# Kernel optimization log

Hardware: AMD Instinct MI355X
Metric: run time of the kernel (lower is better)

The kernel has to match this reference:

```python
import jax, jax.numpy as jnp
import numpy as np

NOISE_STD = 0.1
TOP_K = 2

def setup_inputs() -> dict:
    key = jax.random.key(0)
    k1, k2, k3, k4 = jax.random.split(key, 4)
    B, S, H = 4, 4096, 2048
    E, SE, NS = 64, 64, 10
    x = jax.random.normal(k1, (B, S, H), dtype=jnp.float32)
    scale_embeddings = jax.random.normal(k2, (NS, SE), dtype=jnp.float32)
    # nn.Linear(H+SE, E, bias=False) weight: [E, H+SE]
    router_w = jax.random.normal(k3, (E, H + SE), dtype=jnp.float32) / np.sqrt(H + SE).astype(np.float32)
    # pre-sampled standard-normal noise (training path), scaled by NOISE_STD inside reference
    noise = jax.random.normal(k4, (B, S, E), dtype=jnp.float32)
    return {"x": x, "scale_embeddings": scale_embeddings, "router_w": router_w,
            "noise": noise, "scale_idx": 3}

def reference(x, scale_embeddings, router_w, noise, scale_idx):
    B, S, _ = x.shape
    # scale_idx is not None branch: lookup one scale embedding, broadcast over tokens
    emb = scale_embeddings[scale_idx]                      # [SE]
    emb = jnp.broadcast_to(emb, (B, S, emb.shape[-1]))     # [B,S,SE]
    x_with_scale = jnp.concatenate([x, emb], axis=-1)      # [B,S,H+SE]
    # router: bias-free linear projection to expert logits
    router_logits = jnp.einsum('bsd,ed->bse', x_with_scale, router_w)
    router_logits = router_logits + noise * NOISE_STD      # training noise injection
    routing_probs = jax.nn.softmax(router_logits, axis=-1)  # [B,S,E]
    routing_weights, selected_experts = jax.lax.top_k(routing_probs, TOP_K)
    routing_weights = routing_weights / routing_weights.sum(axis=-1, keepdims=True)
    # scatter normalized weights into dense dispatch tensor [B,S,E]
    dispatch = (jax.nn.one_hot(selected_experts, routing_probs.shape[-1],
                               dtype=routing_probs.dtype)
                * routing_weights[..., None]).sum(axis=-2)
    return dispatch
```

## Files before the change

kernel.cpp:

```cpp
#include <hip/hip_runtime.h>
#include <hip/hip_bf16.h>
#include <math.h>
#include <stdint.h>


#define H_DIM 2048
#define K_TOTAL 2112
#define E_DIM 64
#define SE_DIM 64
#define NSTEP 64
#define TPB 32
#define NBLOCKS (16384 / TPB)
#define STEP_BYTES (12 * 1024)
#define WP_TOTAL (NSTEP * STEP_BYTES)
#define MINS(v) ((v) < NSTEP ? (v) : (NSTEP - 1))

typedef float  f32x4 __attribute__((ext_vector_type(4)));
typedef short  s16x8 __attribute__((ext_vector_type(8)));
typedef unsigned int u32x4 __attribute__((ext_vector_type(4)));

typedef uint32_t __attribute__((address_space(1))) gu32_t;
typedef uint32_t __attribute__((address_space(3))) lu32_t;
__device__ __forceinline__ void gload_lds16(const void* g, void* l) {
    __builtin_amdgcn_global_load_lds((const gu32_t*)g, (lu32_t*)l, 16, 0, 0);
}

__device__ __forceinline__ unsigned short bf16_rne(float f) {
    uint32_t u = __float_as_uint(f);
    return (unsigned short)((u + 0x7FFFu + ((u >> 16) & 1u)) >> 16);
}
__device__ __forceinline__ float bf16_f32(unsigned short h) {
    return __uint_as_float(((uint32_t)h) << 16);
}
__device__ __forceinline__ uint32_t bits_of_bf2(__hip_bfloat162 h) {
    uint32_t u; __builtin_memcpy(&u, &h, 4); return u;
}

__global__ void prep_kernel(const float* __restrict__ W,
                            const float* __restrict__ se,
                            const int* __restrict__ sidx,
                            unsigned short* __restrict__ Wp,
                            float* __restrict__ tail) {
    if (blockIdx.x == 64) {
        int e = threadIdx.x;
        if (e < 64) {
            const float* emb = se + (*sidx) * SE_DIM;
            float t = 0.f;
            for (int j = 0; j < SE_DIM; ++j)
                t = fmaf(emb[j], W[(size_t)e * K_TOTAL + H_DIM + j], t);
            tail[e] = t;
        }
        return;
    }
    int item = blockIdx.x * 256 + threadIdx.x;
    int lane = item & 63;
    int nt   = (item >> 6) & 3;
    int s    = item >> 8;
    int e     = nt * 16 + (lane & 15);
    int kbase = s * 32 + (lane >> 4) * 8;
    const float* wr = W + (size_t)e * K_TOTAL + kbase;
    unsigned short p0[8], p1[8], p2[8];
    #pragma unroll
    for (int j = 0; j < 8; ++j) {
        float v = wr[j];
        unsigned short a0 = bf16_rne(v);
        float r1 = v - bf16_f32(a0);
        unsigned short a1 = bf16_rne(r1);
        float r2 = r1 - bf16_f32(a1);
        p0[j] = a0; p1[j] = a1; p2[j] = bf16_rne(r2);
    }
    size_t rec = (size_t)s * 12 + nt * 3;
    unsigned short* d0 = Wp + (rec + 0) * 512 + lane * 8;
    unsigned short* d1 = Wp + (rec + 1) * 512 + lane * 8;
    unsigned short* d2 = Wp + (rec + 2) * 512 + lane * 8;
    #pragma unroll
    for (int j = 0; j < 8; ++j) { d0[j] = p0[j]; d1[j] = p1[j]; d2[j] = p2[j]; }
}

__device__ __forceinline__ void split3(const float4 fa, const float4 fb,
                                       s16x8& P0, s16x8& P1, s16x8& P2) {
    float f[8] = {fa.x, fa.y, fa.z, fa.w, fb.x, fb.y, fb.z, fb.w};
    uint32_t d0[4], d1[4], d2[4];
    #pragma unroll
    for (int p = 0; p < 4; ++p) {
        float v0 = f[2 * p], v1 = f[2 * p + 1];
        uint32_t u0 = bits_of_bf2(__float22bfloat162_rn(make_float2(v0, v1)));
        float r0 = v0 - __uint_as_float(u0 << 16);
        float r1 = v1 - __uint_as_float(u0 & 0xffff0000u);
        uint32_t u1 = bits_of_bf2(__float22bfloat162_rn(make_float2(r0, r1)));
        float s0 = r0 - __uint_as_float(u1 << 16);
        float s1 = r1 - __uint_as_float(u1 & 0xffff0000u);
        uint32_t u2 = bits_of_bf2(__float22bfloat162_rn(make_float2(s0, s1)));
        d0[p] = u0; d1[p] = u1; d2[p] = u2;
    }
    u32x4 q0 = {d0[0], d0[1], d0[2], d0[3]};
    u32x4 q1 = {d1[0], d1[1], d1[2], d1[3]};
    u32x4 q2 = {d2[0], d2[1], d2[2], d2[3]};
    __builtin_memcpy(&P0, &q0, 16);
    __builtin_memcpy(&P1, &q1, 16);
    __builtin_memcpy(&P2, &q2, 16);
}

__launch_bounds__(256, 2)
__global__ void router_kernel(const float* __restrict__ x,
                              const unsigned char* __restrict__ Wp,
                              const float* __restrict__ tail_g,
                              const float* __restrict__ noise,
                              float* __restrict__ out) {
    __shared__ __align__(16) unsigned char As[4][4096];
    __shared__ __align__(16) unsigned char Bs[4][STEP_BYTES];
    __shared__ float4 cand2[2][TPB];
    __shared__ float4 res[TPB];

    const int tid  = threadIdx.x;
    const int lane = tid & 63;
    const int wave = __builtin_amdgcn_readfirstlane(tid >> 6);
    const int mt   = wave >> 1;
    const int g    = wave & 1;
    const int tok0 = blockIdx.x * TPB;
    const int row  = lane & 15;
    const int quad = lane >> 4;
    const int c    = row;

    const int stok = tid >> 3;
    const int spos = tid & 7;
    const int schk = spos ^ (stok & 7);
    const float* asrc = x + (size_t)(tok0 + stok) * H_DIM + schk * 4;

    const int abase = (mt * 16 + row) * 128;
    const int aoff0 = abase + (((quad * 2)     ^ (row & 7)) << 4);
    const int aoff1 = abase + (((quad * 2 + 1) ^ (row & 7)) << 4);

    f32x4 acc0 = {0.f, 0.f, 0.f, 0.f}, acc1 = acc0;

    #define ISSUE_SET(s_, d_) do {                                          \
        const unsigned char* _bsrc = Wp + (size_t)(s_) * STEP_BYTES;        \
        gload_lds16(asrc + (size_t)(s_) * 32, &As[d_][tid * 16]);           \
        gload_lds16(_bsrc + (size_t)tid * 16,          &Bs[d_][tid * 16]);          \
        gload_lds16(_bsrc + (size_t)(tid + 256) * 16,  &Bs[d_][(tid + 256) * 16]);  \
        gload_lds16(_bsrc + (size_t)(tid + 512) * 16,  &Bs[d_][(tid + 512) * 16]);  \
    } while (0)

    ISSUE_SET(0, 0);
    ISSUE_SET(1, 1);
    ISSUE_SET(2, 2);

    for (int s = 0; s < NSTEP; ++s) {
        asm volatile("s_waitcnt vmcnt(8)\n\ts_barrier" ::: "memory");

        const int slot = s & 3;
        const float4* ab = (const float4*)&As[slot][0];
        float4 a0 = *(const float4*)((const unsigned char*)ab + aoff0);
        float4 a1 = *(const float4*)((const unsigned char*)ab + aoff1);
        s16x8 A0, A1, A2;
        split3(a0, a1, A0, A1, A2);

        const unsigned char* base = &Bs[slot][g * 6144 + lane * 16];
        #pragma unroll
        for (int nt = 0; nt < 2; ++nt) {
            s16x8 B0 = *(const s16x8*)(base + (nt * 3 + 0) * 1024);
            s16x8 B1 = *(const s16x8*)(base + (nt * 3 + 1) * 1024);
            s16x8 B2 = *(const s16x8*)(base + (nt * 3 + 2) * 1024);
            f32x4 a = nt ? acc1 : acc0;
            a = __builtin_amdgcn_mfma_f32_16x16x32_bf16(A0, B0, a, 0, 0, 0);
            a = __builtin_amdgcn_mfma_f32_16x16x32_bf16(A0, B1, a, 0, 0, 0);
            a = __builtin_amdgcn_mfma_f32_16x16x32_bf16(A1, B0, a, 0, 0, 0);
            a = __builtin_amdgcn_mfma_f32_16x16x32_bf16(A0, B2, a, 0, 0, 0);
            a = __builtin_amdgcn_mfma_f32_16x16x32_bf16(A1, B1, a, 0, 0, 0);
            a = __builtin_amdgcn_mfma_f32_16x16x32_bf16(A2, B0, a, 0, 0, 0);
            if (nt) acc1 = a; else acc0 = a;
        }

        ISSUE_SET(MINS(s + 3), (s + 3) & 3);
    }
    #undef ISSUE_SET

    float tl0 = tail_g[g * 32 + c], tl1 = tail_g[g * 32 + 16 + c];
    #pragma unroll
    for (int r = 0; r < 4; ++r) {
        const int tl = mt * 16 + quad * 4 + r;
        const float* nz = noise + (size_t)(tok0 + tl) * E_DIM + g * 32;
        float v0 = acc0[r] + tl0 + 0.1f * nz[c];
        float v1 = acc1[r] + tl1 + 0.1f * nz[16 + c];
        float V1, V2; int I1, I2;
        if (v1 > v0) { V1 = v1; I1 = g * 32 + 16 + c; V2 = v0; I2 = g * 32 + c; }
        else         { V1 = v0; I1 = g * 32 + c;      V2 = v1; I2 = g * 32 + 16 + c; }
        #pragma unroll
        for (int m = 8; m; m >>= 1) {
            float o1 = __shfl_xor(V1, m, 64); int oi1 = __shfl_xor(I1, m, 64);
            float o2 = __shfl_xor(V2, m, 64); int oi2 = __shfl_xor(I2, m, 64);
            if (o1 > V1 || (o1 == V1 && oi1 < I1)) {
                float nv2; int ni2;
                if (V1 > o2 || (V1 == o2 && I1 < oi2)) { nv2 = V1; ni2 = I1; }
                else                                   { nv2 = o2; ni2 = oi2; }
                V1 = o1; I1 = oi1; V2 = nv2; I2 = ni2;
            } else {
                if (o1 > V2 || (o1 == V2 && oi1 < I2)) { V2 = o1; I2 = oi1; }
            }
        }
        if (c == r)
            cand2[g][tl] = make_float4(V1, __int_as_float(I1), V2, __int_as_float(I2));
    }
    __syncthreads();

    if (tid < TPB) {
        float4 q0 = cand2[0][tid];
        float4 q1 = cand2[1][tid];
        float V1 = q0.x, V2 = q0.z;
        int   I1 = __float_as_int(q0.y), I2 = __float_as_int(q0.w);
        if (q1.x > V1) {
            if (q1.z > V1) { V2 = q1.z; I2 = __float_as_int(q1.w); }
            else           { V2 = V1;   I2 = I1; }
            V1 = q1.x; I1 = __float_as_int(q1.y);
        } else if (q1.x > V2) {
            V2 = q1.x; I2 = __float_as_int(q1.y);
        }
        float d   = expf(V2 - V1);
        float inv = 1.0f / (1.0f + d);
        res[tid] = make_float4(inv, __int_as_float(I1), d * inv, __int_as_float(I2));
    }
    __syncthreads();

    float4* outb = (float4*)out + (size_t)blockIdx.x * (TPB * E_DIM / 4);
    #pragma unroll
    for (int pp = 0; pp < 2; ++pp) {
        int p = tid + pp * 256;
        int t = p >> 4, cc = p & 15;
        float4 rr = res[t];
        int ri1 = __float_as_int(rr.y), ri2 = __float_as_int(rr.w);
        int e = cc * 4;
        float4 o;
        o.x = (e + 0 == ri1) ? rr.x : (e + 0 == ri2) ? rr.z : 0.0f;
        o.y = (e + 1 == ri1) ? rr.x : (e + 1 == ri2) ? rr.z : 0.0f;
        o.z = (e + 2 == ri1) ? rr.x : (e + 2 == ri2) ? rr.z : 0.0f;
        o.w = (e + 3 == ri1) ? rr.x : (e + 3 == ri2) ? rr.z : 0.0f;
        outb[p] = o;
    }
}

extern "C" void kernel_launch(void* const* d_in, const int* in_sizes, int n_in,
                              void* d_out, int out_size, void* d_ws, size_t ws_size,
                              hipStream_t stream) {
    const float* x     = (const float*)d_in[0];
    const float* se    = (const float*)d_in[1];
    const float* W     = (const float*)d_in[2];
    const float* noise = (const float*)d_in[3];
    const int*   sidx  = (const int*)d_in[4];
    float* out = (float*)d_out;

    unsigned short* Wp   = (unsigned short*)d_ws;
    float*          tail = (float*)((char*)d_ws + WP_TOTAL);

    hipLaunchKernelGGL(prep_kernel, dim3(65), dim3(256), 0, stream, W, se, sidx, Wp, tail);
    hipLaunchKernelGGL(router_kernel, dim3(NBLOCKS), dim3(256), 0, stream,
                       x, (const unsigned char*)Wp, tail, noise, out);
}
```

Baseline: 223.9 us.

## Split expert columns across 8 waves and issue prefetch before compute

Doubles the block to 512 threads, so each wave owns one 16-expert column tile instead of two. The A and B staging buffers merge into one 16KB set per stage, loaded with two global-to-LDS loads per thread. The prefetch for step s+3 now goes out right after the barrier instead of after the MFMAs, and the wait count drops to match. Top-2 selection merges four per-wave candidates instead of two. The aim is more parallel waves and better latency hiding, at the cost of more block-wide barriers per token and the same data traffic.

Result: slower. 241.3 us (+7.8%).

```diff
diff --git a/kernel.cpp b/kernel.cpp
--- a/kernel.cpp
+++ b/kernel.cpp
@@ -12,6 +12,7 @@
 #define TPB 32
 #define NBLOCKS (16384 / TPB)
 #define STEP_BYTES (12 * 1024)
+#define SET_BYTES (16 * 1024)
 #define WP_TOTAL (NSTEP * STEP_BYTES)
 #define MINS(v) ((v) < NSTEP ? (v) : (NSTEP - 1))
 
@@ -101,44 +102,49 @@
     __builtin_memcpy(&P2, &q2, 16);
 }
 
-__launch_bounds__(256, 2)
+__launch_bounds__(512, 4)
 __global__ void router_kernel(const float* __restrict__ x,
                               const unsigned char* __restrict__ Wp,
                               const float* __restrict__ tail_g,
                               const float* __restrict__ noise,
                               float* __restrict__ out) {
-    __shared__ __align__(16) unsigned char As[4][4096];
-    __shared__ __align__(16) unsigned char Bs[4][STEP_BYTES];
-    __shared__ float4 cand2[2][TPB];
+    __shared__ __align__(16) unsigned char S[4][SET_BYTES];
+    __shared__ float4 cand[4][TPB];
     __shared__ float4 res[TPB];
 
     const int tid  = threadIdx.x;
     const int lane = tid & 63;
     const int wave = __builtin_amdgcn_readfirstlane(tid >> 6);
-    const int mt   = wave >> 1;
-    const int g    = wave & 1;
+    const int mt   = wave >> 2;
+    const int g    = wave & 3;
     const int tok0 = blockIdx.x * TPB;
     const int row  = lane & 15;
     const int quad = lane >> 4;
     const int c    = row;
 
-    const int stok = tid >> 3;
-    const int spos = tid & 7;
-    const int schk = spos ^ (stok & 7);
-    const float* asrc = x + (size_t)(tok0 + stok) * H_DIM + schk * 4;
+    const char* s1; size_t str1;
+    if (tid < 256) {
+        int st = tid >> 3, sp = tid & 7;
+        s1 = (const char*)(x + (size_t)(tok0 + st) * H_DIM + ((sp ^ (st & 7)) << 2));
+        str1 = 128;
+    } else {
+        s1 = (const char*)Wp + (size_t)(tid - 256) * 16;
+        str1 = STEP_BYTES;
+    }
+    const char* s2 = (const char*)Wp + (size_t)(tid + 256) * 16;
+    const int d1 = tid * 16;
+    const int d2 = tid * 16 + 8192;
 
     const int abase = (mt * 16 + row) * 128;
     const int aoff0 = abase + (((quad * 2)     ^ (row & 7)) << 4);
     const int aoff1 = abase + (((quad * 2 + 1) ^ (row & 7)) << 4);
-
-    f32x4 acc0 = {0.f, 0.f, 0.f, 0.f}, acc1 = acc0;
-
-    #define ISSUE_SET(s_, d_) do {                                          \
-        const unsigned char* _bsrc = Wp + (size_t)(s_) * STEP_BYTES;        \
-        gload_lds16(asrc + (size_t)(s_) * 32, &As[d_][tid * 16]);           \
-        gload_lds16(_bsrc + (size_t)tid * 16,          &Bs[d_][tid * 16]);          \
-        gload_lds16(_bsrc + (size_t)(tid + 256) * 16,  &Bs[d_][(tid + 256) * 16]);  \
-        gload_lds16(_bsrc + (size_t)(tid + 512) * 16,  &Bs[d_][(tid + 512) * 16]);  \
+    const int boff  = 4096 + g * 3072 + lane * 16;
+
+    f32x4 acc = {0.f, 0.f, 0.f, 0.f};
+
+    #define ISSUE_SET(s_, d_) do {                                  \
+        gload_lds16(s1 + (size_t)(s_) * str1,       &S[d_][d1]);    \
+        gload_lds16(s2 + (size_t)(s_) * STEP_BYTES, &S[d_][d2]);    \
     } while (0)
 
     ISSUE_SET(0, 0);
@@ -146,45 +152,37 @@
     ISSUE_SET(2, 2);
 
     for (int s = 0; s < NSTEP; ++s) {
-        asm volatile("s_waitcnt vmcnt(8)\n\ts_barrier" ::: "memory");
-
-        const int slot = s & 3;
-        const float4* ab = (const float4*)&As[slot][0];
-        float4 a0 = *(const float4*)((const unsigned char*)ab + aoff0);
-        float4 a1 = *(const float4*)((const unsigned char*)ab + aoff1);
+        asm volatile("s_waitcnt vmcnt(4)\n\ts_barrier" ::: "memory");
+
+        ISSUE_SET(MINS(s + 3), (s + 3) & 3);
+
+        const unsigned char* sb = &S[s & 3][0];
+        float4 a0 = *(const float4*)(sb + aoff0);
+        float4 a1 = *(const float4*)(sb + aoff1);
         s16x8 A0, A1, A2;
         split3(a0, a1, A0, A1, A2);
 
-        const unsigned char* base = &Bs[slot][g * 6144 + lane * 16];
-        #pragma unroll
-        for (int nt = 0; nt < 2; ++nt) {
-            s16x8 B0 = *(const s16x8*)(base + (nt * 3 + 0) * 1024);
-            s16x8 B1 = *(const s16x8*)(base + (nt * 3 + 1) * 1024);
-            s16x8 B2 = *(const s16x8*)(base + (nt * 3 + 2) * 1024);
-            f32x4 a = nt ? acc1 : acc0;
-            a = __builtin_amdgcn_mfma_f32_16x16x32_bf16(A0, B0, a, 0, 0, 0);
-            a = __builtin_amdgcn_mfma_f32_16x16x32_bf16(A0, B1, a, 0, 0, 0);
-            a = __builtin_amdgcn_mfma_f32_16x16x32_bf16(A1, B0, a, 0, 0, 0);
-            a = __builtin_amdgcn_mfma_f32_16x16x32_bf16(A0, B2, a, 0, 0, 0);
-            a = __builtin_amdgcn_mfma_f32_16x16x32_bf16(A1, B1, a, 0, 0, 0);
-            a = __builtin_amdgcn_mfma_f32_16x16x32_bf16(A2, B0, a, 0, 0, 0);
-            if (nt) acc1 = a; else acc0 = a;
-        }
-
-        ISSUE_SET(MINS(s + 3), (s + 3) & 3);
+        const unsigned char* bb = sb + boff;
+        s16x8 B0 = *(const s16x8*)(bb);
+        s16x8 B1 = *(const s16x8*)(bb + 1024);
+        s16x8 B2 = *(const s16x8*)(bb + 2048);
+        acc = __builtin_amdgcn_mfma_f32_16x16x32_bf16(A0, B0, acc, 0, 0, 0);
+        acc = __builtin_amdgcn_mfma_f32_16x16x32_bf16(A0, B1, acc, 0, 0, 0);
+        acc = __builtin_amdgcn_mfma_f32_16x16x32_bf16(A1, B0, acc, 0, 0, 0);
+        acc = __builtin_amdgcn_mfma_f32_16x16x32_bf16(A0, B2, acc, 0, 0, 0);
+        acc = __builtin_amdgcn_mfma_f32_16x16x32_bf16(A1, B1, acc, 0, 0, 0);
+        acc = __builtin_amdgcn_mfma_f32_16x16x32_bf16(A2, B0, acc, 0, 0, 0);
     }
     #undef ISSUE_SET
 
-    float tl0 = tail_g[g * 32 + c], tl1 = tail_g[g * 32 + 16 + c];
+    float tl = tail_g[g * 16 + c];
     #pragma unroll
     for (int r = 0; r < 4; ++r) {
-        const int tl = mt * 16 + quad * 4 + r;
-        const float* nz = noise + (size_t)(tok0 + tl) * E_DIM + g * 32;
-        float v0 = acc0[r] + tl0 + 0.1f * nz[c];
-        float v1 = acc1[r] + tl1 + 0.1f * nz[16 + c];
-        float V1, V2; int I1, I2;
-        if (v1 > v0) { V1 = v1; I1 = g * 32 + 16 + c; V2 = v0; I2 = g * 32 + c; }
-        else         { V1 = v0; I1 = g * 32 + c;      V2 = v1; I2 = g * 32 + 16 + c; }
+        const int tlk = mt * 16 + quad * 4 + r;
+        const float* nz = noise + (size_t)(tok0 + tlk) * E_DIM + g * 16;
+        float v = acc[r] + tl + 0.1f * nz[c];
+        float V1 = v, V2 = -3.4e38f;
+        int   I1 = g * 16 + c, I2 = 0x7fffffff;
         #pragma unroll
         for (int m = 8; m; m >>= 1) {
             float o1 = __shfl_xor(V1, m, 64); int oi1 = __shfl_xor(I1, m, 64);
@@ -199,21 +197,26 @@
             }
         }
         if (c == r)
-            cand2[g][tl] = make_float4(V1, __int_as_float(I1), V2, __int_as_float(I2));
+            cand[g][tlk] = make_float4(V1, __int_as_float(I1), V2, __int_as_float(I2));
     }
     __syncthreads();
 
     if (tid < TPB) {
-        float4 q0 = cand2[0][tid];
-        float4 q1 = cand2[1][tid];
+        float4 q0 = cand[0][tid];
         float V1 = q0.x, V2 = q0.z;
         int   I1 = __float_as_int(q0.y), I2 = __float_as_int(q0.w);
-        if (q1.x > V1) {
-            if (q1.z > V1) { V2 = q1.z; I2 = __float_as_int(q1.w); }
-            else           { V2 = V1;   I2 = I1; }
-            V1 = q1.x; I1 = __float_as_int(q1.y);
-        } else if (q1.x > V2) {
-            V2 = q1.x; I2 = __float_as_int(q1.y);
+        #pragma unroll
+        for (int j = 1; j < 4; ++j) {
+            float4 qj = cand[j][tid];
+            float o1 = qj.x, o2 = qj.z;
+            int  oi1 = __float_as_int(qj.y), oi2 = __float_as_int(qj.w);
+            if (o1 > V1) {
+                if (o2 > V1) { V2 = o2; I2 = oi2; }
+                else         { V2 = V1; I2 = I1;  }
+                V1 = o1; I1 = oi1;
+            } else if (o1 > V2) {
+                V2 = o1; I2 = oi1;
+            }
         }
         float d   = expf(V2 - V1);
         float inv = 1.0f / (1.0f + d);
@@ -222,10 +225,8 @@
     __syncthreads();
 
     float4* outb = (float4*)out + (size_t)blockIdx.x * (TPB * E_DIM / 4);
-    #pragma unroll
-    for (int pp = 0; pp < 2; ++pp) {
-        int p = tid + pp * 256;
-        int t = p >> 4, cc = p & 15;
+    {
+        int t = tid >> 4, cc = tid & 15;
         float4 rr = res[t];
         int ri1 = __float_as_int(rr.y), ri2 = __float_as_int(rr.w);
         int e = cc * 4;
@@ -234,7 +235,7 @@
         o.y = (e + 1 == ri1) ? rr.x : (e + 1 == ri2) ? rr.z : 0.0f;
         o.z = (e + 2 == ri1) ? rr.x : (e + 2 == ri2) ? rr.z : 0.0f;
         o.w = (e + 3 == ri1) ? rr.x : (e + 3 == ri2) ? rr.z : 0.0f;
-        outb[p] = o;
+        outb[tid] = o;
     }
 }
 
@@ -252,6 +253,6 @@
     float*          tail = (float*)((char*)d_ws + WP_TOTAL);
 
     hipLaunchKernelGGL(prep_kernel, dim3(65), dim3(256), 0, stream, W, se, sidx, Wp, tail);
-    hipLaunchKernelGGL(router_kernel, dim3(NBLOCKS), dim3(256), 0, stream,
+    hipLaunchKernelGGL(router_kernel, dim3(NBLOCKS), dim3(512), 0, stream,
                        x, (const unsigned char*)Wp, tail, noise, out);
 }
```

## Restructure LDS pipeline into three-slot ring with split-phase loads and setprio

Applied to the files above, without the earlier changes.

Replaces the four-deep separate A/B LDS buffers with a three-slot combined ring and splits each K-step into two phases. The second weight half is issued after the first MFMA group, with barriers and waitcnts placed between the phases. The weight prepack reorders N-tiles so that each phase reads a contiguous region. It also raises wave priority around the MFMA chains, aiming to cut LDS footprint for occupancy and to overlap loads with compute more finely. The cost is an extra barrier per step and a shallower prefetch depth.

After: 279.2 us. 1.25x slower.

```diff
diff --git a/kernel.cpp b/kernel.cpp
--- a/kernel.cpp
+++ b/kernel.cpp
@@ -12,6 +12,7 @@
 #define TPB 32
 #define NBLOCKS (16384 / TPB)
 #define STEP_BYTES (12 * 1024)
+#define SET_BYTES (16 * 1024)
 #define WP_TOTAL (NSTEP * STEP_BYTES)
 #define MINS(v) ((v) < NSTEP ? (v) : (NSTEP - 1))
 
@@ -69,7 +70,8 @@
         float r2 = r1 - bf16_f32(a1);
         p0[j] = a0; p1[j] = a1; p2[j] = bf16_rne(r2);
     }
-    size_t rec = (size_t)s * 12 + nt * 3;
+    int slot = ((nt & 1) << 1) | (nt >> 1);
+    size_t rec = (size_t)s * 12 + slot * 3;
     unsigned short* d0 = Wp + (rec + 0) * 512 + lane * 8;
     unsigned short* d1 = Wp + (rec + 1) * 512 + lane * 8;
     unsigned short* d2 = Wp + (rec + 2) * 512 + lane * 8;
@@ -107,8 +109,7 @@
                               const float* __restrict__ tail_g,
                               const float* __restrict__ noise,
                               float* __restrict__ out) {
-    __shared__ __align__(16) unsigned char As[4][4096];
-    __shared__ __align__(16) unsigned char Bs[4][STEP_BYTES];
+    __shared__ __align__(16) unsigned char S[3][SET_BYTES];
     __shared__ float4 cand2[2][TPB];
     __shared__ float4 res[TPB];
 
@@ -126,6 +127,7 @@
     const int spos = tid & 7;
     const int schk = spos ^ (stok & 7);
     const float* asrc = x + (size_t)(tok0 + stok) * H_DIM + schk * 4;
+    const unsigned char* bsrc = Wp + (size_t)tid * 16;
 
     const int abase = (mt * 16 + row) * 128;
     const int aoff0 = abase + (((quad * 2)     ^ (row & 7)) << 4);
@@ -133,47 +135,66 @@
 
     f32x4 acc0 = {0.f, 0.f, 0.f, 0.f}, acc1 = acc0;
 
-    #define ISSUE_SET(s_, d_) do {                                          \
-        const unsigned char* _bsrc = Wp + (size_t)(s_) * STEP_BYTES;        \
-        gload_lds16(asrc + (size_t)(s_) * 32, &As[d_][tid * 16]);           \
-        gload_lds16(_bsrc + (size_t)tid * 16,          &Bs[d_][tid * 16]);          \
-        gload_lds16(_bsrc + (size_t)(tid + 256) * 16,  &Bs[d_][(tid + 256) * 16]);  \
-        gload_lds16(_bsrc + (size_t)(tid + 512) * 16,  &Bs[d_][(tid + 512) * 16]);  \
+    #define ISSUE_P0(s_, d_) do {                                       \
+        const unsigned char* _b = bsrc + (size_t)(s_) * STEP_BYTES;     \
+        gload_lds16(asrc + (size_t)(s_) * 32, &S[d_][tid * 16]);        \
+        gload_lds16(_b,        &S[d_][4096 + tid * 16]);                \
+        gload_lds16(_b + 4096, &S[d_][8192 + tid * 16]);                \
     } while (0)
-
-    ISSUE_SET(0, 0);
-    ISSUE_SET(1, 1);
-    ISSUE_SET(2, 2);
-
+    #define ISSUE_P1(s_, d_)                                            \
+        gload_lds16(bsrc + (size_t)(s_) * STEP_BYTES + 8192,            \
+                    &S[d_][12288 + tid * 16])
+
+    ISSUE_P0(0, 0); ISSUE_P1(0, 0);
+    ISSUE_P0(1, 1); ISSUE_P1(1, 1);
+
+    int rd = 0, wr = 2;
     for (int s = 0; s < NSTEP; ++s) {
-        asm volatile("s_waitcnt vmcnt(8)\n\ts_barrier" ::: "memory");
-
-        const int slot = s & 3;
-        const float4* ab = (const float4*)&As[slot][0];
-        float4 a0 = *(const float4*)((const unsigned char*)ab + aoff0);
-        float4 a1 = *(const float4*)((const unsigned char*)ab + aoff1);
+        asm volatile("s_waitcnt vmcnt(5)\n\ts_barrier" ::: "memory");
+        ISSUE_P0(MINS(s + 2), wr);
+
+        const unsigned char* sb = &S[rd][0];
+        float4 a0 = *(const float4*)(sb + aoff0);
+        float4 a1 = *(const float4*)(sb + aoff1);
         s16x8 A0, A1, A2;
         split3(a0, a1, A0, A1, A2);
-
-        const unsigned char* base = &Bs[slot][g * 6144 + lane * 16];
-        #pragma unroll
-        for (int nt = 0; nt < 2; ++nt) {
-            s16x8 B0 = *(const s16x8*)(base + (nt * 3 + 0) * 1024);
-            s16x8 B1 = *(const s16x8*)(base + (nt * 3 + 1) * 1024);
-            s16x8 B2 = *(const s16x8*)(base + (nt * 3 + 2) * 1024);
-            f32x4 a = nt ? acc1 : acc0;
-            a = __builtin_amdgcn_mfma_f32_16x16x32_bf16(A0, B0, a, 0, 0, 0);
-            a = __builtin_amdgcn_mfma_f32_16x16x32_bf16(A0, B1, a, 0, 0, 0);
-            a = __builtin_amdgcn_mfma_f32_16x16x32_bf16(A1, B0, a, 0, 0, 0);
-            a = __builtin_amdgcn_mfma_f32_16x16x32_bf16(A0, B2, a, 0, 0, 0);
-            a = __builtin_amdgcn_mfma_f32_16x16x32_bf16(A1, B1, a, 0, 0, 0);
-            a = __builtin_amdgcn_mfma_f32_16x16x32_bf16(A2, B0, a, 0, 0, 0);
-            if (nt) acc1 = a; else acc0 = a;
-        }
-
-        ISSUE_SET(MINS(s + 3), (s + 3) & 3);
-    }
-    #undef ISSUE_SET
+        {
+            const unsigned char* bb = sb + 4096 + g * 3072 + lane * 16;
+            s16x8 B0 = *(const s16x8*)(bb);
+            s16x8 B1 = *(const s16x8*)(bb + 1024);
+            s16x8 B2 = *(const s16x8*)(bb + 2048);
+            __builtin_amdgcn_s_setprio(1);
+            acc0 = __builtin_amdgcn_mfma_f32_16x16x32_bf16(A0, B0, acc0, 0, 0, 0);
+            acc0 = __builtin_amdgcn_mfma_f32_16x16x32_bf16(A0, B1, acc0, 0, 0, 0);
+            acc0 = __builtin_amdgcn_mfma_f32_16x16x32_bf16(A1, B0, acc0, 0, 0, 0);
+            acc0 = __builtin_amdgcn_mfma_f32_16x16x32_bf16(A0, B2, acc0, 0, 0, 0);
+            acc0 = __builtin_amdgcn_mfma_f32_16x16x32_bf16(A1, B1, acc0, 0, 0, 0);
+            acc0 = __builtin_amdgcn_mfma_f32_16x16x32_bf16(A2, B0, acc0, 0, 0, 0);
+            __builtin_amdgcn_s_setprio(0);
+        }
+
+        asm volatile("s_waitcnt vmcnt(7)\n\ts_barrier" ::: "memory");
+        ISSUE_P1(MINS(s + 2), wr);
+        {
+            const unsigned char* bb = sb + 10240 + g * 3072 + lane * 16;
+            s16x8 B0 = *(const s16x8*)(bb);
+            s16x8 B1 = *(const s16x8*)(bb + 1024);
+            s16x8 B2 = *(const s16x8*)(bb + 2048);
+            __builtin_amdgcn_s_setprio(1);
+            acc1 = __builtin_amdgcn_mfma_f32_16x16x32_bf16(A0, B0, acc1, 0, 0, 0);
+            acc1 = __builtin_amdgcn_mfma_f32_16x16x32_bf16(A0, B1, acc1, 0, 0, 0);
+            acc1 = __builtin_amdgcn_mfma_f32_16x16x32_bf16(A1, B0, acc1, 0, 0, 0);
+            acc1 = __builtin_amdgcn_mfma_f32_16x16x32_bf16(A0, B2, acc1, 0, 0, 0);
+            acc1 = __builtin_amdgcn_mfma_f32_16x16x32_bf16(A1, B1, acc1, 0, 0, 0);
+            acc1 = __builtin_amdgcn_mfma_f32_16x16x32_bf16(A2, B0, acc1, 0, 0, 0);
+            __builtin_amdgcn_s_setprio(0);
+        }
+
+        rd = (rd == 2) ? 0 : rd + 1;
+        wr = (wr == 2) ? 0 : wr + 1;
+    }
+    #undef ISSUE_P0
+    #undef ISSUE_P1
 
     float tl0 = tail_g[g * 32 + c], tl1 = tail_g[g * 32 + 16 + c];
     #pragma unroll
```

## Replace LDS-staged pipeline with direct global-to-register double-buffered loads, 64 tokens/block

Applied to the files above, without the earlier changes.

Removes the shared-memory staging of x and packed weights via global_load_lds with barriers. Each wave now loads its A and B fragments straight from global memory into registers, double-buffered across two steps. The block grows to 512 threads covering 64 tokens. This drops LDS traffic and per-step barriers, but each wave re-reads the weight fragments from global/L2 rather than sharing one LDS copy, and register pressure rises. Some of the hidden epilogue code is sized from TPB and was not visibly adjusted for 8 waves, so consistency is uncertain.

Result: slower. 252.1 us (+12.6%).

```diff
diff --git a/kernel.cpp b/kernel.cpp
--- a/kernel.cpp
+++ b/kernel.cpp
@@ -9,7 +9,7 @@
 #define E_DIM 64
 #define SE_DIM 64
 #define NSTEP 64
-#define TPB 32
+#define TPB 64
 #define NBLOCKS (16384 / TPB)
 #define STEP_BYTES (12 * 1024)
 #define WP_TOTAL (NSTEP * STEP_BYTES)
@@ -18,12 +18,6 @@
 typedef float  f32x4 __attribute__((ext_vector_type(4)));
 typedef short  s16x8 __attribute__((ext_vector_type(8)));
 typedef unsigned int u32x4 __attribute__((ext_vector_type(4)));
-
-typedef uint32_t __attribute__((address_space(1))) gu32_t;
-typedef uint32_t __attribute__((address_space(3))) lu32_t;
-__device__ __forceinline__ void gload_lds16(const void* g, void* l) {
-    __builtin_amdgcn_global_load_lds((const gu32_t*)g, (lu32_t*)l, 16, 0, 0);
-}
 
 __device__ __forceinline__ unsigned short bf16_rne(float f) {
     uint32_t u = __float_as_uint(f);
@@ -101,14 +95,47 @@
     __builtin_memcpy(&P2, &q2, 16);
 }
 
-__launch_bounds__(256, 2)
+struct Frag {
+    float4 a0, a1;
+    s16x8  b0, b1, b2, b3, b4, b5;
+};
+
+__device__ __forceinline__ void load_set(const float* ap,
+                                         const unsigned char* bp, Frag& f) {
+    f.a0 = *(const float4*)(ap);
+    f.a1 = *(const float4*)(ap + 4);
+    f.b0 = *(const s16x8*)(bp);
+    f.b1 = *(const s16x8*)(bp + 1024);
+    f.b2 = *(const s16x8*)(bp + 2048);
+    f.b3 = *(const s16x8*)(bp + 3072);
+    f.b4 = *(const s16x8*)(bp + 4096);
+    f.b5 = *(const s16x8*)(bp + 5120);
+}
+
+__device__ __forceinline__ void step_compute(const Frag& f,
+                                             f32x4& acc0, f32x4& acc1) {
+    s16x8 A0, A1, A2;
+    split3(f.a0, f.a1, A0, A1, A2);
+    acc0 = __builtin_amdgcn_mfma_f32_16x16x32_bf16(A0, f.b0, acc0, 0, 0, 0);
+    acc0 = __builtin_amdgcn_mfma_f32_16x16x32_bf16(A0, f.b1, acc0, 0, 0, 0);
+    acc0 = __builtin_amdgcn_mfma_f32_16x16x32_bf16(A1, f.b0, acc0, 0, 0, 0);
+    acc0 = __builtin_amdgcn_mfma_f32_16x16x32_bf16(A0, f.b2, acc0, 0, 0, 0);
+    acc0 = __builtin_amdgcn_mfma_f32_16x16x32_bf16(A1, f.b1, acc0, 0, 0, 0);
+    acc0 = __builtin_amdgcn_mfma_f32_16x16x32_bf16(A2, f.b0, acc0, 0, 0, 0);
+    acc1 = __builtin_amdgcn_mfma_f32_16x16x32_bf16(A0, f.b3, acc1, 0, 0, 0);
+    acc1 = __builtin_amdgcn_mfma_f32_16x16x32_bf16(A0, f.b4, acc1, 0, 0, 0);
+    acc1 = __builtin_amdgcn_mfma_f32_16x16x32_bf16(A1, f.b3, acc1, 0, 0, 0);
+    acc1 = __builtin_amdgcn_mfma_f32_16x16x32_bf16(A0, f.b5, acc1, 0, 0, 0);
+    acc1 = __builtin_amdgcn_mfma_f32_16x16x32_bf16(A1, f.b4, acc1, 0, 0, 0);
+    acc1 = __builtin_amdgcn_mfma_f32_16x16x32_bf16(A2, f.b3, acc1, 0, 0, 0);
+}
+
+__launch_bounds__(512, 2)
 __global__ void router_kernel(const float* __restrict__ x,
                               const unsigned char* __restrict__ Wp,
                               const float* __restrict__ tail_g,
                               const float* __restrict__ noise,
                               float* __restrict__ out) {
-    __shared__ __align__(16) unsigned char As[4][4096];
-    __shared__ __align__(16) unsigned char Bs[4][STEP_BYTES];
     __shared__ float4 cand2[2][TPB];
     __shared__ float4 res[TPB];
 
@@ -122,58 +149,23 @@
     const int quad = lane >> 4;
     const int c    = row;
 
-    const int stok = tid >> 3;
-    const int spos = tid & 7;
-    const int schk = spos ^ (stok & 7);
-    const float* asrc = x + (size_t)(tok0 + stok) * H_DIM + schk * 4;
-
-    const int abase = (mt * 16 + row) * 128;
-    const int aoff0 = abase + (((quad * 2)     ^ (row & 7)) << 4);
-    const int aoff1 = abase + (((quad * 2 + 1) ^ (row & 7)) << 4);
+    const float* ap = x + (size_t)(tok0 + mt * 16 + row) * H_DIM + quad * 8;
+    const unsigned char* bp = Wp + (size_t)g * 6144 + lane * 16;
 
     f32x4 acc0 = {0.f, 0.f, 0.f, 0.f}, acc1 = acc0;
 
-    #define ISSUE_SET(s_, d_) do {                                          \
-        const unsigned char* _bsrc = Wp + (size_t)(s_) * STEP_BYTES;        \
-        gload_lds16(asrc + (size_t)(s_) * 32, &As[d_][tid * 16]);           \
-        gload_lds16(_bsrc + (size_t)tid * 16,          &Bs[d_][tid * 16]);          \
-        gload_lds16(_bsrc + (size_t)(tid + 256) * 16,  &Bs[d_][(tid + 256) * 16]);  \
-        gload_lds16(_bsrc + (size_t)(tid + 512) * 16,  &Bs[d_][(tid + 512) * 16]);  \
-    } while (0)
-
-    ISSUE_SET(0, 0);
-    ISSUE_SET(1, 1);
-    ISSUE_SET(2, 2);
-
-    for (int s = 0; s < NSTEP; ++s) {
-        asm volatile("s_waitcnt vmcnt(8)\n\ts_barrier" ::: "memory");
-
-        const int slot = s & 3;
-        const float4* ab = (const float4*)&As[slot][0];
-        float4 a0 = *(const float4*)((const unsigned char*)ab + aoff0);
-        float4 a1 = *(const float4*)((const unsigned char*)ab + aoff1);
-        s16x8 A0, A1, A2;
-        split3(a0, a1, A0, A1, A2);
-
-        const unsigned char* base = &Bs[slot][g * 6144 + lane * 16];
-        #pragma unroll
-        for (int nt = 0; nt < 2; ++nt) {
-            s16x8 B0 = *(const s16x8*)(base + (nt * 3 + 0) * 1024);
-            s16x8 B1 = *(const s16x8*)(base + (nt * 3 + 1) * 1024);
-            s16x8 B2 = *(const s16x8*)(base + (nt * 3 + 2) * 1024);
-            f32x4 a = nt ? acc1 : acc0;
-            a = __builtin_amdgcn_mfma_f32_16x16x32_bf16(A0, B0, a, 0, 0, 0);
-            a = __builtin_amdgcn_mfma_f32_16x16x32_bf16(A0, B1, a, 0, 0, 0);
-            a = __builtin_amdgcn_mfma_f32_16x16x32_bf16(A1, B0, a, 0, 0, 0);
-            a = __builtin_amdgcn_mfma_f32_16x16x32_bf16(A0, B2, a, 0, 0, 0);
-            a = __builtin_amdgcn_mfma_f32_16x16x32_bf16(A1, B1, a, 0, 0, 0);
-            a = __builtin_amdgcn_mfma_f32_16x16x32_bf16(A2, B0, a, 0, 0, 0);
-            if (nt) acc1 = a; else acc0 = a;
-        }
-
-        ISSUE_SET(MINS(s + 3), (s + 3) & 3);
-    }
-    #undef ISSUE_SET
+    Frag f0, f1;
+    load_set(ap, bp, f0);
+    #pragma unroll 1
+    for (int s = 0; s < NSTEP; s += 2) {
+        load_set(ap + (size_t)(s + 1) * 32,
+                 bp + (size_t)(s + 1) * STEP_BYTES, f1);
+        step_compute(f0, acc0, acc1);
+        const int s2 = MINS(s + 2);
+        load_set(ap + (size_t)s2 * 32,
+                 bp + (size_t)s2 * STEP_BYTES, f0);
+        step_compute(f1, acc0, acc1);
+    }
 
     float tl0 = tail_g[g * 32 + c], tl1 = tail_g[g * 32 + 16 + c];
     #pragma unroll
@@ -224,7 +216,7 @@
     float4* outb = (float4*)out + (size_t)blockIdx.x * (TPB * E_DIM / 4);
     #pragma unroll
     for (int pp = 0; pp < 2; ++pp) {
-        int p = tid + pp * 256;
+        int p = tid + pp * 512;
         int t = p >> 4, cc = p & 15;
         float4 rr = res[t];
         int ri1 = __float_as_int(rr.y), ri2 = __float_as_int(rr.w);
@@ -252,6 +244,6 @@
     float*          tail = (float*)((char*)d_ws + WP_TOTAL);
 
     hipLaunchKernelGGL(prep_kernel, dim3(65), dim3(256), 0, stream, W, se, sidx, Wp, tail);
-    hipLaunchKernelGGL(router_kernel, dim3(NBLOCKS), dim3(256), 0, stream,
+    hipLaunchKernelGGL(router_kernel, dim3(NBLOCKS), dim3(512), 0, stream,
                        x, (const unsigned char*)Wp, tail, noise, out);
 }
```
